# Optimization experiments

Measured on AMD Instinct MI355X. Metric: run time of the kernel, lower is better.

## Reference

```python
import jax, jax.numpy as jnp
import numpy as np

CLAMP = 1000.0


def setup_inputs() -> dict:
    key = jax.random.key(0)
    k1, k2 = jax.random.split(key)
    B, C, H, W = 1, 32, 160, 320
    left = jax.random.normal(k1, (B, C, H, W), dtype=jnp.float32)
    right = jax.random.normal(k2, (B, C, H, W), dtype=jnp.float32)
    return {"left": left, "right": right, "num_disparities": 64}


def reference(left, right, num_disparities):
    # Left cost volume (is_right=False):
    #   out[b,c,d,h,w] = left[b,c,h,w] * right[b,c,h,w-d]  if w >= d else 0
    orig_dtype = left.dtype
    l = left.astype(jnp.float32)
    r = right.astype(jnp.float32)
    B, C, H, W = l.shape
    d = jnp.arange(num_disparities)[:, None]          # (D, 1)
    w = jnp.arange(W)[None, :]                        # (1, W)
    idx = w - d                                       # (D, W)
    valid = idx >= 0                                  # (D, W)
    # Gather shifted right features: (B, C, H, D, W) -> (B, C, D, H, W)
    rg = r[..., jnp.clip(idx, 0, W - 1)]
    rg = jnp.transpose(rg, (0, 1, 3, 2, 4))
    vol = l[:, :, None, :, :] * rg                    # (B, C, D, H, W)
    vol = jnp.where(valid[None, None, :, None, :], vol, jnp.float32(0))
    return jnp.clip(vol, -CLAMP, CLAMP).astype(orig_dtype)
```

## Files before the change

kernel.cpp:

```cpp
#include <hip/hip_runtime.h>


constexpr float CLAMPV = 1000.0f;
constexpr int C  = 32;
constexpr int H  = 160;
constexpr int W  = 320;
constexpr int W4 = W / 4;
constexpr int BLOCK = 256;

typedef float fx4 __attribute__((ext_vector_type(4)));

__global__ __launch_bounds__(BLOCK) void costvol_kernel(
    const float* __restrict__ left,
    const float* __restrict__ right,
    float* __restrict__ out,
    int D)
{
    const int ch = blockIdx.x;
    const int c  = ch / H;
    const int h  = ch - c * H;

    __shared__ float sL[W];
    __shared__ float sR[W];

    const float* lrow = left  + (size_t)ch * W;
    const float* rrow = right + (size_t)ch * W;

    const int t = threadIdx.x;
    if (t < W4) {
        reinterpret_cast<fx4*>(sL)[t] =
            reinterpret_cast<const fx4*>(lrow)[t];
    } else if (t < 2 * W4) {
        reinterpret_cast<fx4*>(sR)[t - W4] =
            reinterpret_cast<const fx4*>(rrow)[t - W4];
    }
    __syncthreads();

    float* obase = out + ((size_t)c * D * H + h) * W;

    const int total = D * W4;
    for (int idx = t; idx < total; idx += BLOCK) {
        const int d  = idx / W4;
        const int w4 = idx - d * W4;
        const int w  = w4 * 4;

        const fx4 l = reinterpret_cast<const fx4*>(sL)[w4];

        const int i0 = w - d;
        const float r0 = (i0     >= 0) ? sR[i0]     : 0.0f;
        const float r1 = (i0 + 1 >= 0) ? sR[i0 + 1] : 0.0f;
        const float r2 = (i0 + 2 >= 0) ? sR[i0 + 2] : 0.0f;
        const float r3 = (i0 + 3 >= 0) ? sR[i0 + 3] : 0.0f;

        fx4 o;
        o.x = fminf(fmaxf(l.x * r0, -CLAMPV), CLAMPV);
        o.y = fminf(fmaxf(l.y * r1, -CLAMPV), CLAMPV);
        o.z = fminf(fmaxf(l.z * r2, -CLAMPV), CLAMPV);
        o.w = fminf(fmaxf(l.w * r3, -CLAMPV), CLAMPV);

        *reinterpret_cast<fx4*>(obase + (size_t)d * H * W + w) = o;
    }
}

extern "C" void kernel_launch(void* const* d_in, const int* in_sizes, int n_in,
                              void* d_out, int out_size, void* d_ws, size_t ws_size,
                              hipStream_t stream) {
    const float* left  = (const float*)d_in[0];
    const float* right = (const float*)d_in[1];
    float* out = (float*)d_out;

    const int D = out_size / in_sizes[0];

    dim3 grid(C * H, 1, 1);
    dim3 block(BLOCK, 1, 1);
    costvol_kernel<<<grid, block, 0, stream>>>(left, right, out, D);
}
```

Measured before the change: 87.90 us.

## Specialize cost volume kernel for D=64 with register-held left and aligned shared loads

Adds a D=64 specialized kernel that keeps the left row in registers (five fx4 per thread, since 256 mod 80 cycles through fixed w offsets), stores the right row zero-padded in shared memory, and builds the shifted right vector from two aligned fx4 loads plus select logic. This drops the per-element bounds checks and scalar shared loads. Both kernels now write with nontemporal stores to avoid polluting cache with the large write-only output. The generic path is kept for other D values.

```diff
diff --git a/kernel.cpp b/kernel.cpp
--- a/kernel.cpp
+++ b/kernel.cpp
@@ -1,16 +1,98 @@
 #include <hip/hip_runtime.h>
 
+
+typedef float fx4 __attribute__((ext_vector_type(4)));
 
 constexpr float CLAMPV = 1000.0f;
 constexpr int C  = 32;
 constexpr int H  = 160;
 constexpr int W  = 320;
-constexpr int W4 = W / 4;
+constexpr int W4 = 80;
 constexpr int BLOCK = 256;
+constexpr int PADF4 = 16;
+constexpr int SRP = PADF4 + W4 + 1;
 
-typedef float fx4 __attribute__((ext_vector_type(4)));
+__device__ __forceinline__ fx4 clamp4(fx4 l, fx4 r) {
+    fx4 o;
+    o.x = fminf(fmaxf(l.x * r.x, -CLAMPV), CLAMPV);
+    o.y = fminf(fmaxf(l.y * r.y, -CLAMPV), CLAMPV);
+    o.z = fminf(fmaxf(l.z * r.z, -CLAMPV), CLAMPV);
+    o.w = fminf(fmaxf(l.w * r.w, -CLAMPV), CLAMPV);
+    return o;
+}
 
-__global__ __launch_bounds__(BLOCK) void costvol_kernel(
+__device__ __forceinline__ fx4 wsel(const fx4 A, const fx4 B, const int o) {
+    const bool o2 = (o & 2) != 0, o1 = (o & 1) != 0;
+    const float t0 = o2 ? A.z : A.x;
+    const float t1 = o2 ? A.w : A.y;
+    const float t2 = o2 ? B.x : A.z;
+    const float t3 = o2 ? B.y : A.w;
+    const float t4 = o2 ? B.z : B.x;
+    fx4 r;
+    r.x = o1 ? t1 : t0;
+    r.y = o1 ? t2 : t1;
+    r.z = o1 ? t3 : t2;
+    r.w = o1 ? t4 : t3;
+    return r;
+}
+
+__global__ __launch_bounds__(BLOCK) void costvol64(
+    const float* __restrict__ left,
+    const float* __restrict__ right,
+    float* __restrict__ out)
+{
+    constexpr int D = 64;
+    const int ch = blockIdx.x;
+    const int c  = ch / H;
+    const int h  = ch - c * H;
+
+    __shared__ fx4 sRp[SRP];
+
+    const int t = threadIdx.x;
+    const float* lrow = left  + (size_t)ch * W;
+    const float* rrow = right + (size_t)ch * W;
+
+    const int tw = t % W4;
+    fx4 lreg[5];
+    #pragma unroll
+    for (int m = 0; m < 5; ++m) {
+        int w4m = tw + 16 * m; if (w4m >= W4) w4m -= W4;
+        lreg[m] = reinterpret_cast<const fx4*>(lrow)[w4m];
+    }
+
+    if (t < W4) {
+        sRp[PADF4 + t] = reinterpret_cast<const fx4*>(rrow)[t];
+    } else if (t <= W4 + PADF4) {
+        fx4 z = {0.f, 0.f, 0.f, 0.f};
+        sRp[(t == W4 + PADF4) ? (SRP - 1) : (t - W4)] = z;
+    }
+    __syncthreads();
+
+    const fx4* Ab = sRp + PADF4;
+    float* obase = out + ((size_t)c * D * H + h) * W;
+
+    #pragma unroll 1
+    for (int k5 = 0; k5 < 4; ++k5) {
+        #pragma unroll
+        for (int m = 0; m < 5; ++m) {
+            const int k   = k5 * 5 + m;
+            const int idx = t + BLOCK * k;
+            const int d   = idx / W4;
+            const int w4  = idx - d * W4;
+            const int s   = 4 * w4 - d;
+            const int qa  = s >> 2;
+            const int o   = s & 3;
+            const fx4 A = Ab[qa];
+            const fx4 B = Ab[qa + 1];
+            const fx4 r = wsel(A, B, o);
+            const fx4 ov = clamp4(lreg[m], r);
+            __builtin_nontemporal_store(ov,
+                reinterpret_cast<fx4*>(obase + (size_t)d * (H * W) + 4 * w4));
+        }
+    }
+}
+
+__global__ __launch_bounds__(BLOCK) void costvol_generic(
     const float* __restrict__ left,
     const float* __restrict__ right,
     float* __restrict__ out,
@@ -28,37 +110,28 @@
 
     const int t = threadIdx.x;
     if (t < W4) {
-        reinterpret_cast<fx4*>(sL)[t] =
-            reinterpret_cast<const fx4*>(lrow)[t];
+        reinterpret_cast<fx4*>(sL)[t] = reinterpret_cast<const fx4*>(lrow)[t];
     } else if (t < 2 * W4) {
-        reinterpret_cast<fx4*>(sR)[t - W4] =
-            reinterpret_cast<const fx4*>(rrow)[t - W4];
+        reinterpret_cast<fx4*>(sR)[t - W4] = reinterpret_cast<const fx4*>(rrow)[t - W4];
     }
     __syncthreads();
 
     float* obase = out + ((size_t)c * D * H + h) * W;
-
     const int total = D * W4;
     for (int idx = t; idx < total; idx += BLOCK) {
         const int d  = idx / W4;
         const int w4 = idx - d * W4;
         const int w  = w4 * 4;
-
         const fx4 l = reinterpret_cast<const fx4*>(sL)[w4];
-
         const int i0 = w - d;
         const float r0 = (i0     >= 0) ? sR[i0]     : 0.0f;
         const float r1 = (i0 + 1 >= 0) ? sR[i0 + 1] : 0.0f;
         const float r2 = (i0 + 2 >= 0) ? sR[i0 + 2] : 0.0f;
         const float r3 = (i0 + 3 >= 0) ? sR[i0 + 3] : 0.0f;
-
-        fx4 o;
-        o.x = fminf(fmaxf(l.x * r0, -CLAMPV), CLAMPV);
-        o.y = fminf(fmaxf(l.y * r1, -CLAMPV), CLAMPV);
-        o.z = fminf(fmaxf(l.z * r2, -CLAMPV), CLAMPV);
-        o.w = fminf(fmaxf(l.w * r3, -CLAMPV), CLAMPV);
-
-        *reinterpret_cast<fx4*>(obase + (size_t)d * H * W + w) = o;
+        fx4 rr = {r0, r1, r2, r3};
+        const fx4 ov = clamp4(l, rr);
+        __builtin_nontemporal_store(ov,
+            reinterpret_cast<fx4*>(obase + (size_t)d * (H * W) + w));
     }
 }
 
@@ -73,5 +146,9 @@
 
     dim3 grid(C * H, 1, 1);
     dim3 block(BLOCK, 1, 1);
-    costvol_kernel<<<grid, block, 0, stream>>>(left, right, out, D);
+    if (D == 64) {
+        costvol64<<<grid, block, 0, stream>>>(left, right, out);
+    } else {
+        costvol_generic<<<grid, block, 0, stream>>>(left, right, out, D);
+    }
 }
```

New measurement: 83.69 us. -4.8%, faster.
